# Optimization experiments

Measured on AMD Instinct MI355X. Metric: run time of the kernel, lower is better.

Reference implementation:

```python
import jax, jax.numpy as jnp
import numpy as np

jax.config.update("jax_enable_x64", True)  # original casts to double for cov/cholesky

B, C, H, W, DR = 64, 2048, 14, 14, 256
EPS = 1e-6      # LCMCOV eps added to covariance diagonal
BN_EPS = 1e-5   # torch BatchNorm2d default eps


def setup_inputs() -> dict:
    key = jax.random.key(0)
    k0, k1 = jax.random.split(key)
    x = jax.random.normal(k0, (B, C, H, W), dtype=jnp.float32)
    # 1x1 conv weight (kaiming fan_out for relu): std = sqrt(2 / fan_out), fan_out = DR*1*1... torch uses fan_out = out_ch*k*k per output; approximate with sqrt(2/C) scale on (DR, C)
    w_conv = jax.random.normal(k1, (DR, C), dtype=jnp.float32) * np.sqrt(2.0 / C).astype(np.float32)
    gamma = jnp.ones((DR,), jnp.float32)
    beta = jnp.zeros((DR,), jnp.float32)
    run_mean = jnp.zeros((DR,), jnp.float32)
    run_var = jnp.ones((DR,), jnp.float32)
    return {"x": x, "w_conv": w_conv, "gamma": gamma, "beta": beta,
            "run_mean": run_mean, "run_var": run_var}


def reference(x, w_conv, gamma, beta, run_mean, run_var):
    b, c, h, w = x.shape
    dr = w_conv.shape[0]
    m = h * w
    # 1x1 conv (no bias) + BatchNorm2d (eval mode, running stats) + ReLU
    y = jnp.einsum('bchw,dc->bdhw', x, w_conv)
    scale = gamma / jnp.sqrt(run_var + BN_EPS)
    y = y * scale[None, :, None, None] + (beta - run_mean * scale)[None, :, None, None]
    y = jax.nn.relu(y)
    # Covpool in float64: x I_hat x^T == (1/M) * (x - mean)(x - mean)^T
    xd = y.reshape(b, dr, m).astype(jnp.float64)
    xc = xd - xd.mean(axis=2, keepdims=True)  # [B, DR, M]
    cov = jnp.einsum('bdm,bem->bde', xc, xc) / m  # [B, DR, DR]
    # LogI_LCM: Cholesky, log the diagonal, symmetrize
    cov = cov + EPS * jnp.eye(dr, dtype=jnp.float64)
    L = jnp.linalg.cholesky(cov)
    diag = jnp.log(jnp.diagonal(L, axis1=-2, axis2=-1))          # [B, DR]
    tril = jnp.tril(L, -1) + jnp.eye(dr, dtype=L.dtype) * diag[:, :, None]
    sym = tril + jnp.swapaxes(tril, -1, -2)
    # Triuvec: upper-triangular (incl diag) entries in row-major order, cast to float32
    iu, ju = jnp.triu_indices(dr)
    return sym[:, iu, ju].astype(jnp.float32)  # [B, DR*(DR+1)/2]
```

## Files before the change

### kernel.cpp

```cpp
#include <hip/hip_runtime.h>
#include <math.h>

#define BB 64
#define CC 2048
#define MM 196
#define DD 256
#define NTOT (BB * MM)

typedef __attribute__((ext_vector_type(8))) short short8;
typedef __attribute__((ext_vector_type(4))) short short4v;
typedef __attribute__((ext_vector_type(4))) unsigned short ushort4v;
typedef __attribute__((ext_vector_type(4))) float f32x4;

__device__ __forceinline__ unsigned short bf16_rne(float f) {
  unsigned int u = __float_as_uint(f);
  unsigned int r = u + 0x7FFFu + ((u >> 16) & 1u);
  return (unsigned short)(r >> 16);
}

__global__ __launch_bounds__(256) void k_prep(
    const float* __restrict__ w, const float* __restrict__ gamma,
    const float* __restrict__ beta, const float* __restrict__ rmean,
    const float* __restrict__ rvar, unsigned short* __restrict__ wh,
    unsigned short* __restrict__ wl, float* __restrict__ sclv,
    float* __restrict__ sftv) {
  const int e0 = (blockIdx.x * 256 + threadIdx.x) * 4;
  f32x4 v = *(const f32x4*)(w + e0);
  ushort4v h, l;
#pragma unroll
  for (int i = 0; i < 4; ++i) {
    unsigned short hb = bf16_rne(v[i]);
    float hf = __uint_as_float((unsigned int)hb << 16);
    h[i] = hb;
    l[i] = bf16_rne(v[i] - hf);
  }
  *(ushort4v*)(wh + e0) = h;
  *(ushort4v*)(wl + e0) = l;
  if (blockIdx.x == 0 && threadIdx.x < DD) {
    int d = threadIdx.x;
    float s = gamma[d] / sqrtf(rvar[d] + 1e-5f);
    sclv[d] = s;
    sftv[d] = beta[d] - rmean[d] * s;
  }
}

__global__ __launch_bounds__(256, 2) void k_conv(
    const float* __restrict__ x, const unsigned short* __restrict__ wh,
    const unsigned short* __restrict__ wl, const float* __restrict__ sclv,
    const float* __restrict__ sftv, float* __restrict__ yt) {
  const int tid = threadIdx.x;
  const int wid = tid >> 6, lane = tid & 63;
  const int quad = lane >> 4, l16 = lane & 15;
  const int n0 = blockIdx.x * 64;

  __shared__ unsigned short Xh[2][64][36];
  __shared__ unsigned short Xl[2][64][36];

  f32x4 acc[4][4];
#pragma unroll
  for (int i = 0; i < 4; ++i)
#pragma unroll
    for (int j = 0; j < 4; ++j) acc[i][j] = (f32x4)0.f;

  const int nX = tid & 63, kq = tid >> 6;
  const int gn = n0 + nX;
  const int bX = gn / MM, mX = gn - bX * MM;
  const float* xp = x + (size_t)bX * CC * MM + mX;

  size_t aoff[4];
#pragma unroll
  for (int ds = 0; ds < 4; ++ds)
    aoff[ds] = (size_t)(wid * 64 + ds * 16 + l16) * CC + quad * 8;

  short8 Ah[4], Al[4], Ah2[4], Al2[4];
#pragma unroll
  for (int ds = 0; ds < 4; ++ds) {
    Ah[ds] = *(const short8*)(wh + aoff[ds]);
    Al[ds] = *(const short8*)(wl + aoff[ds]);
  }

  float xr[8];
#pragma unroll
  for (int p = 0; p < 8; ++p) xr[p] = xp[(size_t)(kq * 8 + p) * MM];
  {
    ushort4v h0, h1, l0, l1;
#pragma unroll
    for (int p = 0; p < 4; ++p) {
      unsigned short hb = bf16_rne(xr[p]);
      float hf = __uint_as_float((unsigned int)hb << 16);
      h0[p] = hb;
      l0[p] = bf16_rne(xr[p] - hf);
    }
#pragma unroll
    for (int p = 0; p < 4; ++p) {
      unsigned short hb = bf16_rne(xr[4 + p]);
      float hf = __uint_as_float((unsigned int)hb << 16);
      h1[p] = hb;
      l1[p] = bf16_rne(xr[4 + p] - hf);
    }
    *(ushort4v*)&Xh[0][nX][kq * 8] = h0;
    *(ushort4v*)&Xh[0][nX][kq * 8 + 4] = h1;
    *(ushort4v*)&Xl[0][nX][kq * 8] = l0;
    *(ushort4v*)&Xl[0][nX][kq * 8 + 4] = l1;
  }
#pragma unroll
  for (int p = 0; p < 8; ++p) xr[p] = xp[(size_t)(32 + kq * 8 + p) * MM];
  __syncthreads();

  for (int c = 0; c < 64; ++c) {
    const int buf = c & 1;
    if (c < 63) {
      ushort4v h0, h1, l0, l1;
#pragma unroll
      for (int p = 0; p < 4; ++p) {
        unsigned short hb = bf16_rne(xr[p]);
        float hf = __uint_as_float((unsigned int)hb << 16);
        h0[p] = hb;
        l0[p] = bf16_rne(xr[p] - hf);
      }
#pragma unroll
      for (int p = 0; p < 4; ++p) {
        unsigned short hb = bf16_rne(xr[4 + p]);
        float hf = __uint_as_float((unsigned int)hb << 16);
        h1[p] = hb;
        l1[p] = bf16_rne(xr[4 + p] - hf);
      }
      *(ushort4v*)&Xh[buf ^ 1][nX][kq * 8] = h0;
      *(ushort4v*)&Xh[buf ^ 1][nX][kq * 8 + 4] = h1;
      *(ushort4v*)&Xl[buf ^ 1][nX][kq * 8] = l0;
      *(ushort4v*)&Xl[buf ^ 1][nX][kq * 8 + 4] = l1;
      if (c < 62) {
#pragma unroll
        for (int p = 0; p < 8; ++p)
          xr[p] = xp[(size_t)((c + 2) * 32 + kq * 8 + p) * MM];
      }
#pragma unroll
      for (int ds = 0; ds < 4; ++ds) {
        Ah2[ds] = *(const short8*)(wh + aoff[ds] + (c + 1) * 32);
        Al2[ds] = *(const short8*)(wl + aoff[ds] + (c + 1) * 32);
      }
    }
#pragma unroll
    for (int ns = 0; ns < 4; ++ns) {
      const unsigned short* bp = &Xh[buf][ns * 16 + l16][quad * 8];
      short4v b0 = *(const short4v*)bp;
      short4v b1 = *(const short4v*)(bp + 4);
      short8 Bh = __builtin_shufflevector(b0, b1, 0, 1, 2, 3, 4, 5, 6, 7);
      const unsigned short* bq = &Xl[buf][ns * 16 + l16][quad * 8];
      short4v c0 = *(const short4v*)bq;
      short4v c1 = *(const short4v*)(bq + 4);
      short8 Bl = __builtin_shufflevector(c0, c1, 0, 1, 2, 3, 4, 5, 6, 7);
#pragma unroll
      for (int ds = 0; ds < 4; ++ds) {
        acc[ds][ns] = __builtin_amdgcn_mfma_f32_16x16x32_bf16(
            Ah[ds], Bh, acc[ds][ns], 0, 0, 0);
        acc[ds][ns] = __builtin_amdgcn_mfma_f32_16x16x32_bf16(
            Ah[ds], Bl, acc[ds][ns], 0, 0, 0);
        acc[ds][ns] = __builtin_amdgcn_mfma_f32_16x16x32_bf16(
            Al[ds], Bh, acc[ds][ns], 0, 0, 0);
      }
    }
    __syncthreads();
    if (c < 63) {
#pragma unroll
      for (int ds = 0; ds < 4; ++ds) {
        Ah[ds] = Ah2[ds];
        Al[ds] = Al2[ds];
      }
    }
  }

#pragma unroll
  for (int ds = 0; ds < 4; ++ds) {
    const int dbase = wid * 64 + ds * 16 + quad * 4;
    f32x4 s4 = *(const f32x4*)(sclv + dbase);
    f32x4 f4 = *(const f32x4*)(sftv + dbase);
#pragma unroll
    for (int ns = 0; ns < 4; ++ns) {
      const int n = n0 + ns * 16 + l16;
      const int b = n / MM, m = n - b * MM;
      f32x4 o;
#pragma unroll
      for (int r = 0; r < 4; ++r) {
        float v = fmaf(acc[ds][ns][r], s4[r], f4[r]);
        o[r] = v > 0.f ? v : 0.f;
      }
      *(f32x4*)(yt + ((size_t)b * MM + m) * DD + dbase) = o;
    }
  }
}

__global__ __launch_bounds__(256) void k_cov(const float* __restrict__ yt,
                                             double* __restrict__ cov) {
  const int b = blockIdx.x;
  const int t = blockIdx.y;
  const int ti = (t < 1) ? 0 : (t < 3) ? 1 : (t < 6) ? 2 : 3;
  const int tj = t - (ti * (ti + 1)) / 2;
  const int i0 = ti * 64, j0 = tj * 64;
  const int tid = threadIdx.x;
  const int tx = tid & 15, ty = tid >> 4;

  __shared__ double As[32][66];
  __shared__ double Bs[32][66];
  __shared__ double Ms[4][64];

  double acc[4][4];
#pragma unroll
  for (int i = 0; i < 4; ++i)
#pragma unroll
    for (int j = 0; j < 4; ++j) acc[i][j] = 0.0;

  const int dl = tid & 63, kl = tid >> 6;
  const float* ybase = yt + (size_t)b * MM * DD;

  {
    const int base_d = ((kl < 2) ? i0 : j0) + dl;
    const int mlo = (kl & 1) ? 98 : 0;
    const int mhi = (kl & 1) ? 196 : 98;
    double s = 0.0;
    for (int m = mlo; m < mhi; ++m)
      s += (double)ybase[(size_t)m * DD + base_d];
    Ms[kl][dl] = s;
  }
  __syncthreads();
  const double mA = (Ms[0][dl] + Ms[1][dl]) * (1.0 / MM);
  const double mB = (Ms[2][dl] + Ms[3][dl]) * (1.0 / MM);

  for (int k0 = 0; k0 < MM; k0 += 32) {
    __syncthreads();
#pragma unroll
    for (int p = 0; p < 8; ++p) {
      int k = kl + p * 4;
      int m = k0 + k;
      double av = 0.0, bv = 0.0;
      if (m < MM) {
        av = (double)ybase[(size_t)m * DD + i0 + dl] - mA;
        bv = (double)ybase[(size_t)m * DD + j0 + dl] - mB;
      }
      As[k][dl] = av;
      Bs[k][dl] = bv;
    }
    __syncthreads();
#pragma unroll
    for (int k = 0; k < 32; ++k) {
      double a[4], bv[4];
#pragma unroll
      for (int i = 0; i < 4; ++i) a[i] = As[k][ty * 4 + i];
#pragma unroll
      for (int j = 0; j < 4; ++j) bv[j] = Bs[k][tx * 4 + j];
#pragma unroll
      for (int i = 0; i < 4; ++i)
#pragma unroll
        for (int j = 0; j < 4; ++j) acc[i][j] = fma(a[i], bv[j], acc[i][j]);
    }
  }

  double* cb = cov + (size_t)b * DD * DD;
#pragma unroll
  for (int i = 0; i < 4; ++i) {
#pragma unroll
    for (int j = 0; j < 4; ++j) {
      int gi = i0 + ty * 4 + i, gj = j0 + tx * 4 + j;
      double v = acc[i][j] * (1.0 / MM);
      if (gi == gj) v += 1e-6;
      cb[(size_t)gi * DD + gj] = v;
      if (ti != tj) cb[(size_t)gj * DD + gi] = v;
    }
  }
}

__global__ __launch_bounds__(256) void k_panel3(double* __restrict__ cov,
                                                int kb) {
  const int b = blockIdx.x;
  double* A = cov + (size_t)b * DD * DD;
  const int j0 = kb * 32;
  const int tid = threadIdx.x;

  __shared__ double sh[4224];

  if (blockIdx.y == 0) {
    double(*LpTop)[33] = (double(*)[33])sh;
    double(*L11s)[33] = (double(*)[33])(sh + 1056);
    double* rpivs = sh + 2112;
    const int R = DD - j0;
    const int pj = j0 - 32;

    double sp[32];
    const double* rowp = A + (size_t)(j0 + tid) * DD;
    if (tid < R) {
#pragma unroll
      for (int c = 0; c < 32; ++c) sp[c] = rowp[j0 + c];
    }

    if (kb > 0) {
      double lp[32];
      if (tid < R) {
#pragma unroll
        for (int c = 0; c < 32; ++c) lp[c] = rowp[pj + c];
      }
      if (tid < 32) {
#pragma unroll
        for (int c = 0; c < 32; ++c) LpTop[tid][c] = lp[c];
      }
      __syncthreads();
      if (tid < R) {
#pragma unroll
        for (int c = 0; c < 32; ++c) {
          double a = 0.0;
#pragma unroll
          for (int p = 0; p < 32; ++p) a = fma(lp[p], LpTop[c][p], a);
          sp[c] -= a;
        }
      }
    }

    if (tid < 32) {
      double rpkeep = 0.0;
#pragma unroll
      for (int j = 0; j < 32; ++j) {
        double dj = __shfl(sp[j], j);
        double piv = sqrt(dj);
        double rp = 1.0 / piv;
        if (tid == j) {
          sp[j] = piv;
          rpkeep = rp;
        } else {
          sp[j] = sp[j] * rp;
        }
        double lij = sp[j];
#pragma unroll
        for (int k = j + 1; k < 32; ++k) {
          double ck = __shfl(lij, k);
          sp[k] -= lij * ck;
        }
      }
#pragma unroll
      for (int k = 0; k < 32; ++k) L11s[tid][k] = (k <= tid) ? sp[k] : 0.0;
      rpivs[tid] = rpkeep;
      for (int k = 0; k <= tid; ++k)
        A[(size_t)(j0 + tid) * DD + j0 + k] = sp[k];
    }
    __syncthreads();

    if (tid >= 32 && tid < R) {
#pragma unroll
      for (int j = 0; j < 32; ++j) {
        double s = sp[j];
#pragma unroll
        for (int k = 0; k < 32; ++k)
          if (k < j) s -= sp[k] * L11s[j][k];
        sp[j] = s * rpivs[j];
      }
      double* dst = A + (size_t)(j0 + tid) * DD + j0;
#pragma unroll
      for (int k = 0; k < 32; ++k) dst[k] = sp[k];
    }
  } else {
    const int o = j0 + 32;
    const int S = DD - o;
    const int pj = j0 - 32;
    int tI = 0, tJ = (int)blockIdx.y - 1;
    while (tJ > tI) {
      tJ -= (tI + 1);
      tI++;
    }
    const int i0 = tI * 64, jj0 = tJ * 64;
    const int txl = tid & 15, tyl = tid >> 4;

    double(*Ea)[33] = (double(*)[33])sh;
    double(*Eb)[33] = (double(*)[33])(sh + 2112);

    for (int e = tid; e < 64 * 32; e += 256) {
      int r = e >> 5, c = e & 31;
      Ea[r][c] = (i0 + r < S) ? A[(size_t)(o + i0 + r) * DD + pj + c] : 0.0;
      Eb[r][c] = (jj0 + r < S) ? A[(size_t)(o + jj0 + r) * DD + pj + c] : 0.0;
    }
    __syncthreads();

    double s[4][4];
#pragma unroll
    for (int i = 0; i < 4; ++i)
#pragma unroll
      for (int j = 0; j < 4; ++j) s[i][j] = 0.0;

    const int bi = tyl * 4, bj = txl * 4;
#pragma unroll
    for (int k = 0; k < 32; ++k) {
      double a[4], bv[4];
#pragma unroll
      for (int i = 0; i < 4; ++i) a[i] = Ea[bi + i][k];
#pragma unroll
      for (int j = 0; j < 4; ++j) bv[j] = Eb[bj + j][k];
#pragma unroll
      for (int i = 0; i < 4; ++i)
#pragma unroll
        for (int j = 0; j < 4; ++j) s[i][j] = fma(a[i], bv[j], s[i][j]);
    }

#pragma unroll
    for (int i = 0; i < 4; ++i)
#pragma unroll
      for (int j = 0; j < 4; ++j) {
        int gi = i0 + bi + i, gj = jj0 + bj + j;
        if (gi < S && gj < S && gi >= gj)
          A[(size_t)(o + gi) * DD + (o + gj)] -= s[i][j];
      }
  }
}

__global__ __launch_bounds__(256) void k_out(const double* __restrict__ cov,
                                             float* __restrict__ out) {
  const int b = blockIdx.y;
  int t = blockIdx.x;
  int ti = 0, tj = t;
  while (tj >= 4 - ti) {
    tj -= (4 - ti);
    ti++;
  }
  tj += ti;
  const int tid = threadIdx.x;
  const double* A = cov + (size_t)b * DD * DD;

  __shared__ float S[64][65];
  for (int e = tid; e < 4096; e += 256) {
    int jj = e >> 6, ii = e & 63;
    S[jj][ii] = (float)A[(size_t)(tj * 64 + jj) * DD + ti * 64 + ii];
  }
  __syncthreads();

  for (int e = tid; e < 4096; e += 256) {
    int ii = e >> 6, jj = e & 63;
    int i = ti * 64 + ii, j = tj * 64 + jj;
    if (j < i) continue;
    float v = S[jj][ii];
    if (i == j) v = 2.0f * logf(v);
    int off = i * DD - (i * (i - 1)) / 2 + (j - i);
    out[(size_t)b * 32896 + off] = v;
  }
}

extern "C" void kernel_launch(void* const* d_in, const int* in_sizes, int n_in,
                              void* d_out, int out_size, void* d_ws,
                              size_t ws_size, hipStream_t stream) {
  const float* x = (const float*)d_in[0];
  const float* w = (const float*)d_in[1];
  const float* gamma = (const float*)d_in[2];
  const float* beta = (const float*)d_in[3];
  const float* rmean = (const float*)d_in[4];
  const float* rvar = (const float*)d_in[5];
  float* out = (float*)d_out;

  char* ws = (char*)d_ws;
  float* yt = (float*)ws;
  double* cov = (double*)(ws + 12845056 + 131072);
  unsigned short* wh = (unsigned short*)cov;
  unsigned short* wl = wh + (DD * CC);
  float* sclv = (float*)(wl + (DD * CC));
  float* sftv = sclv + DD;

  k_prep<<<512, 256, 0, stream>>>(w, gamma, beta, rmean, rvar, wh, wl, sclv,
                                  sftv);
  k_conv<<<NTOT / 64, 256, 0, stream>>>(x, wh, wl, sclv, sftv, yt);
  k_cov<<<dim3(BB, 10), 256, 0, stream>>>(yt, cov);
  for (int kb = 0; kb < 8; ++kb) {
    int ntiles = 0;
    if (kb > 0) {
      int S = DD - (kb * 32 + 32);
      if (S > 0) {
        int nt = (S + 63) / 64;
        ntiles = nt * (nt + 1) / 2;
      }
    }
    k_panel3<<<dim3(BB, 1 + ntiles), 256, 0, stream>>>(cov, kb);
  }
  k_out<<<dim3(10, BB), 256, 0, stream>>>(cov, out);
}
```

Baseline: 604.5 us.

## Widen blocked Cholesky panels to 64 columns and cut kernel launches

Replaces the eight 32-column panel steps with four 64-column steps. Each panel is staged in a large shared-memory tile and factored there as two 32-column sub-panels with an in-block update between them. The trailing update then uses rank-64 tiles. This halves the number of dependent launches and gives the trailing GEMM more arithmetic per load. In exchange the single panel block does more serial work and uses much more shared memory (about 150KB), which limits occupancy.

```diff
diff --git a/kernel.cpp b/kernel.cpp
--- a/kernel.cpp
+++ b/kernel.cpp
@@ -269,96 +269,183 @@
   }
 }
 
-__global__ __launch_bounds__(256) void k_panel3(double* __restrict__ cov,
-                                                int kb) {
+__global__ __launch_bounds__(256) void k_panel64(double* __restrict__ cov,
+                                                 int s) {
   const int b = blockIdx.x;
   double* A = cov + (size_t)b * DD * DD;
-  const int j0 = kb * 32;
+  const int j0 = s * 64;
   const int tid = threadIdx.x;
 
-  __shared__ double sh[4224];
+  __shared__ double Sp[256][65];
+  __shared__ double Aux[2112];
 
   if (blockIdx.y == 0) {
-    double(*LpTop)[33] = (double(*)[33])sh;
-    double(*L11s)[33] = (double(*)[33])(sh + 1056);
-    double* rpivs = sh + 2112;
     const int R = DD - j0;
-    const int pj = j0 - 32;
-
-    double sp[32];
-    const double* rowp = A + (size_t)(j0 + tid) * DD;
-    if (tid < R) {
-#pragma unroll
-      for (int c = 0; c < 32; ++c) sp[c] = rowp[j0 + c];
-    }
-
-    if (kb > 0) {
-      double lp[32];
-      if (tid < R) {
-#pragma unroll
-        for (int c = 0; c < 32; ++c) lp[c] = rowp[pj + c];
-      }
-      if (tid < 32) {
-#pragma unroll
-        for (int c = 0; c < 32; ++c) LpTop[tid][c] = lp[c];
-      }
-      __syncthreads();
-      if (tid < R) {
-#pragma unroll
-        for (int c = 0; c < 32; ++c) {
-          double a = 0.0;
-#pragma unroll
-          for (int p = 0; p < 32; ++p) a = fma(lp[p], LpTop[c][p], a);
-          sp[c] -= a;
-        }
-      }
-    }
+    const int pj = j0 - 64;
+
+    for (int e = tid; e < R * 64; e += 256) {
+      int r = e >> 6, c = e & 63;
+      Sp[r][c] = A[(size_t)(j0 + r) * DD + j0 + c];
+    }
+
+    if (s > 0) {
+      double(*LpTop)[33] = (double(*)[33])Aux;
+      for (int kk = 0; kk < 64; kk += 32) {
+        __syncthreads();
+        for (int e = tid; e < 64 * 32; e += 256) {
+          int r = e >> 5, p = e & 31;
+          LpTop[r][p] = A[(size_t)(j0 + r) * DD + pj + kk + p];
+        }
+        __syncthreads();
+        if (tid < R) {
+          double lp32[32];
+          const double* rowp = A + (size_t)(j0 + tid) * DD + pj + kk;
+#pragma unroll
+          for (int p = 0; p < 32; ++p) lp32[p] = rowp[p];
+#pragma unroll 4
+          for (int c = 0; c < 64; ++c) {
+            double a = 0.0;
+#pragma unroll
+            for (int p = 0; p < 32; ++p) a = fma(lp32[p], LpTop[c][p], a);
+            Sp[tid][c] -= a;
+          }
+        }
+      }
+    }
+    __syncthreads();
+
+    double(*L11s)[33] = (double(*)[33])Aux;
+    double* rpiv = Aux + 1056;
 
     if (tid < 32) {
-      double rpkeep = 0.0;
+      double r[32];
+#pragma unroll
+      for (int k = 0; k < 32; ++k) r[k] = Sp[tid][k];
+      double rpk = 0.0;
 #pragma unroll
       for (int j = 0; j < 32; ++j) {
-        double dj = __shfl(sp[j], j);
+        double dj = __shfl(r[j], j);
         double piv = sqrt(dj);
         double rp = 1.0 / piv;
         if (tid == j) {
-          sp[j] = piv;
-          rpkeep = rp;
+          r[j] = piv;
+          rpk = rp;
         } else {
-          sp[j] = sp[j] * rp;
-        }
-        double lij = sp[j];
+          r[j] = r[j] * rp;
+        }
+        double lij = r[j];
 #pragma unroll
         for (int k = j + 1; k < 32; ++k) {
           double ck = __shfl(lij, k);
-          sp[k] -= lij * ck;
-        }
-      }
-#pragma unroll
-      for (int k = 0; k < 32; ++k) L11s[tid][k] = (k <= tid) ? sp[k] : 0.0;
-      rpivs[tid] = rpkeep;
-      for (int k = 0; k <= tid; ++k)
-        A[(size_t)(j0 + tid) * DD + j0 + k] = sp[k];
-    }
-    __syncthreads();
-
-    if (tid >= 32 && tid < R) {
+          r[k] -= lij * ck;
+        }
+      }
+#pragma unroll
+      for (int k = 0; k < 32; ++k) L11s[tid][k] = (k <= tid) ? r[k] : 0.0;
+      rpiv[tid] = rpk;
+#pragma unroll
+      for (int k = 0; k < 32; ++k)
+        if (k <= tid) Sp[tid][k] = r[k];
+    }
+    __syncthreads();
+
+    {
+      const int T = R - 32;
+      if (tid < T) {
+        double q[32];
+#pragma unroll
+        for (int k = 0; k < 32; ++k) q[k] = Sp[32 + tid][k];
+#pragma unroll
+        for (int j = 0; j < 32; ++j) {
+          double sv = q[j];
+#pragma unroll
+          for (int k = 0; k < 32; ++k)
+            if (k < j) sv -= q[k] * L11s[j][k];
+          q[j] = sv * rpiv[j];
+        }
+#pragma unroll
+        for (int k = 0; k < 32; ++k) Sp[32 + tid][k] = q[k];
+      }
+    }
+    __syncthreads();
+
+    {
+      const int T = R - 32;
+      if (tid < T) {
+        double q[32];
+#pragma unroll
+        for (int p = 0; p < 32; ++p) q[p] = Sp[32 + tid][p];
+#pragma unroll 4
+        for (int c = 0; c < 32; ++c) {
+          double a = 0.0;
+#pragma unroll
+          for (int p = 0; p < 32; ++p) a = fma(q[p], Sp[32 + c][p], a);
+          Sp[32 + tid][32 + c] -= a;
+        }
+      }
+    }
+    __syncthreads();
+
+    if (tid < 32) {
+      double r[32];
+#pragma unroll
+      for (int k = 0; k < 32; ++k) r[k] = Sp[32 + tid][32 + k];
+      double rpk = 0.0;
 #pragma unroll
       for (int j = 0; j < 32; ++j) {
-        double s = sp[j];
-#pragma unroll
-        for (int k = 0; k < 32; ++k)
-          if (k < j) s -= sp[k] * L11s[j][k];
-        sp[j] = s * rpivs[j];
-      }
-      double* dst = A + (size_t)(j0 + tid) * DD + j0;
-#pragma unroll
-      for (int k = 0; k < 32; ++k) dst[k] = sp[k];
+        double dj = __shfl(r[j], j);
+        double piv = sqrt(dj);
+        double rp = 1.0 / piv;
+        if (tid == j) {
+          r[j] = piv;
+          rpk = rp;
+        } else {
+          r[j] = r[j] * rp;
+        }
+        double lij = r[j];
+#pragma unroll
+        for (int k = j + 1; k < 32; ++k) {
+          double ck = __shfl(lij, k);
+          r[k] -= lij * ck;
+        }
+      }
+#pragma unroll
+      for (int k = 0; k < 32; ++k) L11s[tid][k] = (k <= tid) ? r[k] : 0.0;
+      rpiv[tid] = rpk;
+#pragma unroll
+      for (int k = 0; k < 32; ++k)
+        if (k <= tid) Sp[32 + tid][32 + k] = r[k];
+    }
+    __syncthreads();
+
+    {
+      const int T2 = R - 64;
+      if (tid < T2) {
+        double q[32];
+#pragma unroll
+        for (int k = 0; k < 32; ++k) q[k] = Sp[64 + tid][32 + k];
+#pragma unroll
+        for (int j = 0; j < 32; ++j) {
+          double sv = q[j];
+#pragma unroll
+          for (int k = 0; k < 32; ++k)
+            if (k < j) sv -= q[k] * L11s[j][k];
+          q[j] = sv * rpiv[j];
+        }
+#pragma unroll
+        for (int k = 0; k < 32; ++k) Sp[64 + tid][32 + k] = q[k];
+      }
+    }
+    __syncthreads();
+
+    for (int e = tid; e < R * 64; e += 256) {
+      int r = e >> 6, c = e & 63;
+      if (r >= 64 || c <= r) A[(size_t)(j0 + r) * DD + j0 + c] = Sp[r][c];
     }
   } else {
-    const int o = j0 + 32;
+    const int o = j0 + 64;
     const int S = DD - o;
-    const int pj = j0 - 32;
+    const int pj = j0 - 64;
     int tI = 0, tJ = (int)blockIdx.y - 1;
     while (tJ > tI) {
       tJ -= (tI + 1);
@@ -367,25 +454,25 @@
     const int i0 = tI * 64, jj0 = tJ * 64;
     const int txl = tid & 15, tyl = tid >> 4;
 
-    double(*Ea)[33] = (double(*)[33])sh;
-    double(*Eb)[33] = (double(*)[33])(sh + 2112);
-
-    for (int e = tid; e < 64 * 32; e += 256) {
-      int r = e >> 5, c = e & 31;
+    double(*Ea)[65] = (double(*)[65])&Sp[0][0];
+    double(*Eb)[65] = (double(*)[65])&Sp[64][0];
+
+    for (int e = tid; e < 64 * 64; e += 256) {
+      int r = e >> 6, c = e & 63;
       Ea[r][c] = (i0 + r < S) ? A[(size_t)(o + i0 + r) * DD + pj + c] : 0.0;
       Eb[r][c] = (jj0 + r < S) ? A[(size_t)(o + jj0 + r) * DD + pj + c] : 0.0;
     }
     __syncthreads();
 
-    double s[4][4];
+    double acc2[4][4];
 #pragma unroll
     for (int i = 0; i < 4; ++i)
 #pragma unroll
-      for (int j = 0; j < 4; ++j) s[i][j] = 0.0;
+      for (int j = 0; j < 4; ++j) acc2[i][j] = 0.0;
 
     const int bi = tyl * 4, bj = txl * 4;
-#pragma unroll
-    for (int k = 0; k < 32; ++k) {
+#pragma unroll 8
+    for (int k = 0; k < 64; ++k) {
       double a[4], bv[4];
 #pragma unroll
       for (int i = 0; i < 4; ++i) a[i] = Ea[bi + i][k];
@@ -394,7 +481,7 @@
 #pragma unroll
       for (int i = 0; i < 4; ++i)
 #pragma unroll
-        for (int j = 0; j < 4; ++j) s[i][j] = fma(a[i], bv[j], s[i][j]);
+        for (int j = 0; j < 4; ++j) acc2[i][j] = fma(a[i], bv[j], acc2[i][j]);
     }
 
 #pragma unroll
@@ -403,7 +490,7 @@
       for (int j = 0; j < 4; ++j) {
         int gi = i0 + bi + i, gj = jj0 + bj + j;
         if (gi < S && gj < S && gi >= gj)
-          A[(size_t)(o + gi) * DD + (o + gj)] -= s[i][j];
+          A[(size_t)(o + gi) * DD + (o + gj)] -= acc2[i][j];
       }
   }
 }
@@ -462,16 +549,9 @@
                                   sftv);
   k_conv<<<NTOT / 64, 256, 0, stream>>>(x, wh, wl, sclv, sftv, yt);
   k_cov<<<dim3(BB, 10), 256, 0, stream>>>(yt, cov);
-  for (int kb = 0; kb < 8; ++kb) {
-    int ntiles = 0;
-    if (kb > 0) {
-      int S = DD - (kb * 32 + 32);
-      if (S > 0) {
-        int nt = (S + 63) / 64;
-        ntiles = nt * (nt + 1) / 2;
-      }
-    }
-    k_panel3<<<dim3(BB, 1 + ntiles), 256, 0, stream>>>(cov, kb);
+  const int ntr[4] = {0, 3, 1, 0};
+  for (int s = 0; s < 4; ++s) {
+    k_panel64<<<dim3(BB, 1 + ntr[s]), 256, 0, stream>>>(cov, s);
   }
   k_out<<<dim3(10, BB), 256, 0, stream>>>(cov, out);
 }
```

Result: slower. 706.3 us (+16.8%).

## Process two 32-column Cholesky panels per launch with a 64-wide lagged trailing update

Applied to the files above, without the earlier changes.

Replaces the eight per-32-column panel launches with four launches. Each launch factors two consecutive 32-column sub-panels, updating the second sub-panel in-block from shared memory, and applies a 64-deep lagged trailing update to the remaining matrix. This halves the kernel launches and grid-wide synchronisation points in the serial Cholesky chain. In exchange it uses more shared memory per block and puts more serial work in the single panel block.

```diff
diff --git a/kernel.cpp b/kernel.cpp
--- a/kernel.cpp
+++ b/kernel.cpp
@@ -269,96 +269,188 @@
   }
 }
 
-__global__ __launch_bounds__(256) void k_panel3(double* __restrict__ cov,
-                                                int kb) {
+__global__ __launch_bounds__(256) void k_panel2x(double* __restrict__ cov,
+                                                 int t) {
   const int b = blockIdx.x;
   double* A = cov + (size_t)b * DD * DD;
-  const int j0 = kb * 32;
   const int tid = threadIdx.x;
 
-  __shared__ double sh[4224];
+  __shared__ double sh[9536];
+  double(*Lst)[33] = (double(*)[33])sh;
+  double(*LpTop)[33] = (double(*)[33])(sh + 7392);
+  double(*L11s)[33] = (double(*)[33])(sh + 8448);
+  double* rpivs = sh + 9504;
 
   if (blockIdx.y == 0) {
-    double(*LpTop)[33] = (double(*)[33])sh;
-    double(*L11s)[33] = (double(*)[33])(sh + 1056);
-    double* rpivs = sh + 2112;
-    const int R = DD - j0;
-    const int pj = j0 - 32;
-
-    double sp[32];
-    const double* rowp = A + (size_t)(j0 + tid) * DD;
-    if (tid < R) {
-#pragma unroll
-      for (int c = 0; c < 32; ++c) sp[c] = rowp[j0 + c];
-    }
-
-    if (kb > 0) {
-      double lp[32];
+    const int j0a = t * 64;
+    const int pj = j0a - 64;
+
+    {
+      const int j0 = j0a;
+      const int R = DD - j0;
+      double sp[32];
+      const double* rowp = A + (size_t)(j0 + tid) * DD;
       if (tid < R) {
 #pragma unroll
-        for (int c = 0; c < 32; ++c) lp[c] = rowp[pj + c];
+        for (int c = 0; c < 32; ++c) sp[c] = rowp[j0 + c];
+      }
+      if (t > 0) {
+        for (int kk = 0; kk < 64; kk += 32) {
+          double lp[32];
+          if (tid < R) {
+#pragma unroll
+            for (int p = 0; p < 32; ++p) lp[p] = rowp[pj + kk + p];
+          }
+          __syncthreads();
+          if (tid < 32) {
+#pragma unroll
+            for (int p = 0; p < 32; ++p) LpTop[tid][p] = lp[p];
+          }
+          __syncthreads();
+          if (tid < R) {
+#pragma unroll
+            for (int c = 0; c < 32; ++c) {
+              double a = 0.0;
+#pragma unroll
+              for (int p = 0; p < 32; ++p) a = fma(lp[p], LpTop[c][p], a);
+              sp[c] -= a;
+            }
+          }
+        }
       }
       if (tid < 32) {
-#pragma unroll
-        for (int c = 0; c < 32; ++c) LpTop[tid][c] = lp[c];
+        double rpk = 0.0;
+#pragma unroll
+        for (int j = 0; j < 32; ++j) {
+          double dj = __shfl(sp[j], j);
+          double piv = sqrt(dj);
+          double rp = 1.0 / piv;
+          if (tid == j) {
+            sp[j] = piv;
+            rpk = rp;
+          } else {
+            sp[j] = sp[j] * rp;
+          }
+          double lij = sp[j];
+#pragma unroll
+          for (int k = j + 1; k < 32; ++k) {
+            double ck = __shfl(lij, k);
+            sp[k] -= lij * ck;
+          }
+        }
+#pragma unroll
+        for (int k = 0; k < 32; ++k) L11s[tid][k] = (k <= tid) ? sp[k] : 0.0;
+        rpivs[tid] = rpk;
+        for (int k = 0; k <= tid; ++k)
+          A[(size_t)(j0 + tid) * DD + j0 + k] = sp[k];
       }
       __syncthreads();
+      if (tid >= 32 && tid < R) {
+#pragma unroll
+        for (int j = 0; j < 32; ++j) {
+          double s = sp[j];
+#pragma unroll
+          for (int k = 0; k < 32; ++k)
+            if (k < j) s -= sp[k] * L11s[j][k];
+          sp[j] = s * rpivs[j];
+        }
+        double* dst = A + (size_t)(j0 + tid) * DD + j0;
+#pragma unroll
+        for (int k = 0; k < 32; ++k) {
+          dst[k] = sp[k];
+          Lst[tid - 32][k] = sp[k];
+        }
+      }
+      __syncthreads();
+    }
+
+    {
+      const int j0 = j0a + 32;
+      const int R = DD - j0;
+      double sp[32];
+      const double* rowp = A + (size_t)(j0 + tid) * DD;
+      if (tid < R) {
+#pragma unroll
+        for (int c = 0; c < 32; ++c) sp[c] = rowp[j0 + c];
+      }
+      if (t > 0) {
+        for (int kk = 0; kk < 64; kk += 32) {
+          double lp[32];
+          if (tid < R) {
+#pragma unroll
+            for (int p = 0; p < 32; ++p) lp[p] = rowp[pj + kk + p];
+          }
+          __syncthreads();
+          if (tid < 32) {
+#pragma unroll
+            for (int p = 0; p < 32; ++p) LpTop[tid][p] = lp[p];
+          }
+          __syncthreads();
+          if (tid < R) {
+#pragma unroll
+            for (int c = 0; c < 32; ++c) {
+              double a = 0.0;
+#pragma unroll
+              for (int p = 0; p < 32; ++p) a = fma(lp[p], LpTop[c][p], a);
+              sp[c] -= a;
+            }
+          }
+        }
+      }
       if (tid < R) {
 #pragma unroll
         for (int c = 0; c < 32; ++c) {
           double a = 0.0;
 #pragma unroll
-          for (int p = 0; p < 32; ++p) a = fma(lp[p], LpTop[c][p], a);
+          for (int p = 0; p < 32; ++p) a = fma(Lst[tid][p], Lst[c][p], a);
           sp[c] -= a;
         }
       }
-    }
-
-    if (tid < 32) {
-      double rpkeep = 0.0;
-#pragma unroll
-      for (int j = 0; j < 32; ++j) {
-        double dj = __shfl(sp[j], j);
-        double piv = sqrt(dj);
-        double rp = 1.0 / piv;
-        if (tid == j) {
-          sp[j] = piv;
-          rpkeep = rp;
-        } else {
-          sp[j] = sp[j] * rp;
-        }
-        double lij = sp[j];
-#pragma unroll
-        for (int k = j + 1; k < 32; ++k) {
-          double ck = __shfl(lij, k);
-          sp[k] -= lij * ck;
-        }
-      }
-#pragma unroll
-      for (int k = 0; k < 32; ++k) L11s[tid][k] = (k <= tid) ? sp[k] : 0.0;
-      rpivs[tid] = rpkeep;
-      for (int k = 0; k <= tid; ++k)
-        A[(size_t)(j0 + tid) * DD + j0 + k] = sp[k];
-    }
-    __syncthreads();
-
-    if (tid >= 32 && tid < R) {
-#pragma unroll
-      for (int j = 0; j < 32; ++j) {
-        double s = sp[j];
-#pragma unroll
-        for (int k = 0; k < 32; ++k)
-          if (k < j) s -= sp[k] * L11s[j][k];
-        sp[j] = s * rpivs[j];
-      }
-      double* dst = A + (size_t)(j0 + tid) * DD + j0;
-#pragma unroll
-      for (int k = 0; k < 32; ++k) dst[k] = sp[k];
+      if (tid < 32) {
+        double rpk = 0.0;
+#pragma unroll
+        for (int j = 0; j < 32; ++j) {
+          double dj = __shfl(sp[j], j);
+          double piv = sqrt(dj);
+          double rp = 1.0 / piv;
+          if (tid == j) {
+            sp[j] = piv;
+            rpk = rp;
+          } else {
+            sp[j] = sp[j] * rp;
+          }
+          double lij = sp[j];
+#pragma unroll
+          for (int k = j + 1; k < 32; ++k) {
+            double ck = __shfl(lij, k);
+            sp[k] -= lij * ck;
+          }
+        }
+#pragma unroll
+        for (int k = 0; k < 32; ++k) L11s[tid][k] = (k <= tid) ? sp[k] : 0.0;
+        rpivs[tid] = rpk;
+        for (int k = 0; k <= tid; ++k)
+          A[(size_t)(j0 + tid) * DD + j0 + k] = sp[k];
+      }
+      __syncthreads();
+      if (tid >= 32 && tid < R) {
+#pragma unroll
+        for (int j = 0; j < 32; ++j) {
+          double s = sp[j];
+#pragma unroll
+          for (int k = 0; k < 32; ++k)
+            if (k < j) s -= sp[k] * L11s[j][k];
+          sp[j] = s * rpivs[j];
+        }
+        double* dst = A + (size_t)(j0 + tid) * DD + j0;
+#pragma unroll
+        for (int k = 0; k < 32; ++k) dst[k] = sp[k];
+      }
     }
   } else {
-    const int o = j0 + 32;
+    const int o = (t + 1) * 64;
     const int S = DD - o;
-    const int pj = j0 - 32;
+    const int pj2 = (t - 1) * 64;
     int tI = 0, tJ = (int)blockIdx.y - 1;
     while (tJ > tI) {
       tJ -= (tI + 1);
@@ -367,25 +459,25 @@
     const int i0 = tI * 64, jj0 = tJ * 64;
     const int txl = tid & 15, tyl = tid >> 4;
 
-    double(*Ea)[33] = (double(*)[33])sh;
-    double(*Eb)[33] = (double(*)[33])(sh + 2112);
-
-    for (int e = tid; e < 64 * 32; e += 256) {
-      int r = e >> 5, c = e & 31;
-      Ea[r][c] = (i0 + r < S) ? A[(size_t)(o + i0 + r) * DD + pj + c] : 0.0;
-      Eb[r][c] = (jj0 + r < S) ? A[(size_t)(o + jj0 + r) * DD + pj + c] : 0.0;
+    double(*Ea)[65] = (double(*)[65])sh;
+    double(*Eb)[65] = (double(*)[65])(sh + 4160);
+
+    for (int e = tid; e < 64 * 64; e += 256) {
+      int r = e >> 6, c = e & 63;
+      Ea[r][c] = (i0 + r < S) ? A[(size_t)(o + i0 + r) * DD + pj2 + c] : 0.0;
+      Eb[r][c] = (jj0 + r < S) ? A[(size_t)(o + jj0 + r) * DD + pj2 + c] : 0.0;
     }
     __syncthreads();
 
-    double s[4][4];
+    double acc2[4][4];
 #pragma unroll
     for (int i = 0; i < 4; ++i)
 #pragma unroll
-      for (int j = 0; j < 4; ++j) s[i][j] = 0.0;
+      for (int j = 0; j < 4; ++j) acc2[i][j] = 0.0;
 
     const int bi = tyl * 4, bj = txl * 4;
-#pragma unroll
-    for (int k = 0; k < 32; ++k) {
+#pragma unroll 8
+    for (int k = 0; k < 64; ++k) {
       double a[4], bv[4];
 #pragma unroll
       for (int i = 0; i < 4; ++i) a[i] = Ea[bi + i][k];
@@ -394,7 +486,7 @@
 #pragma unroll
       for (int i = 0; i < 4; ++i)
 #pragma unroll
-        for (int j = 0; j < 4; ++j) s[i][j] = fma(a[i], bv[j], s[i][j]);
+        for (int j = 0; j < 4; ++j) acc2[i][j] = fma(a[i], bv[j], acc2[i][j]);
     }
 
 #pragma unroll
@@ -403,7 +495,7 @@
       for (int j = 0; j < 4; ++j) {
         int gi = i0 + bi + i, gj = jj0 + bj + j;
         if (gi < S && gj < S && gi >= gj)
-          A[(size_t)(o + gi) * DD + (o + gj)] -= s[i][j];
+          A[(size_t)(o + gi) * DD + (o + gj)] -= acc2[i][j];
       }
   }
 }
@@ -462,16 +554,9 @@
                                   sftv);
   k_conv<<<NTOT / 64, 256, 0, stream>>>(x, wh, wl, sclv, sftv, yt);
   k_cov<<<dim3(BB, 10), 256, 0, stream>>>(yt, cov);
-  for (int kb = 0; kb < 8; ++kb) {
-    int ntiles = 0;
-    if (kb > 0) {
-      int S = DD - (kb * 32 + 32);
-      if (S > 0) {
-        int nt = (S + 63) / 64;
-        ntiles = nt * (nt + 1) / 2;
-      }
-    }
-    k_panel3<<<dim3(BB, 1 + ntiles), 256, 0, stream>>>(cov, kb);
+  const int ntr[4] = {0, 3, 1, 0};
+  for (int tt = 0; tt < 4; ++tt) {
+    k_panel2x<<<dim3(BB, 1 + ntr[tt]), 256, 0, stream>>>(cov, tt);
   }
   k_out<<<dim3(10, BB), 256, 0, stream>>>(cov, out);
 }
```

Measured after the change: 814.6 us. 1.35x slower.
